# Optimization experiments

Hardware: AMD Instinct MI355X
Metric: run time of the kernel (lower is better)

Reference implementation:

```python
import jax, jax.numpy as jnp
import numpy as np

B, S, H, D = 4, 1024, 16, 64
DIM = H * D          # 1024
FF_INNER = 4 * DIM   # 4096
ROT_BASE = 1000.0


def _l2norm(x):
    # F.normalize(p=2, dim=-1): x / max(||x||_2, 1e-12)
    n = jnp.linalg.norm(x, axis=-1, keepdims=True)
    return x / jnp.maximum(n, 1e-12)


def _rmsnorm(x):
    return x * jax.lax.rsqrt(jnp.mean(x * x, axis=-1, keepdims=True) + jnp.finfo(jnp.float32).eps)


def _rope_tables(seq, d, base):
    inv_freq = base ** (-(jnp.arange(0, d, 2, dtype=jnp.float32) / d))
    freqs = jnp.outer(jnp.arange(seq, dtype=jnp.float32), inv_freq)  # [S, D/2]
    # original caches cos/sin in bfloat16
    cos = jnp.cos(freqs).astype(jnp.bfloat16)[None, :, None, :]
    sin = jnp.sin(freqs).astype(jnp.bfloat16)[None, :, None, :]
    return cos, sin


def _rope(x, cos, sin):
    d = x.shape[3] // 2
    x1, x2 = x[..., :d], x[..., d:]
    y1 = x1 * cos + x2 * sin
    y2 = -x1 * sin + x2 * cos
    return jnp.concatenate([y1, y2], axis=3).astype(x.dtype)


def setup_inputs() -> dict:
    key = jax.random.key(0)
    ks = jax.random.split(key, 12)
    w = lambda k, shp: 0.02 * jax.random.normal(k, shp, dtype=jnp.float32)
    inp = {
        'h_states': jax.random.normal(ks[0], (B, S, DIM), dtype=jnp.float32),
        'attention_mask': jnp.tril(jnp.ones((S, S), dtype=jnp.float32))[None].repeat(B, axis=0),
        'Wq': w(ks[1], (DIM, DIM)), 'Wk': w(ks[2], (DIM, DIM)), 'Wv': w(ks[3], (DIM, DIM)),
        'WqB': w(ks[4], (DIM, DIM)), 'WkB': w(ks[5], (DIM, DIM)),
        'Wo': w(ks[6], (DIM, DIM)), 'bo': jnp.zeros((DIM,), jnp.float32),
        'Wff_in': w(ks[7], (DIM, 2 * FF_INNER)), 'bff_in': jnp.zeros((2 * FF_INNER,), jnp.float32),
        'Wff_out': w(ks[8], (FF_INNER, DIM)), 'bff_out': jnp.zeros((DIM,), jnp.float32),
        'learnedlambda': jnp.asarray(1.0, jnp.float32),
        'l2normscale': jnp.log(jnp.asarray(float(S) ** 2 - float(S), jnp.float32)),
    }
    return inp


def reference(h_states, attention_mask, Wq, Wk, Wv, WqB, WkB, Wo, bo,
              Wff_in, bff_in, Wff_out, bff_out, learnedlambda, l2normscale):
    inner = _rmsnorm(h_states)                               # layerwisenorm (rmsnorm, no affine)
    scale = D ** -0.5

    def proj(Wm):
        return (inner @ Wm).reshape(B, S, H, D)
    q, k, v = proj(Wq), proj(Wk), proj(Wv)
    bq, bk = proj(WqB), proj(WkB)

    cos, sin = _rope_tables(S, D, ROT_BASE)
    q = _rope(_l2norm(q), cos, sin)
    k = _rope(_l2norm(k), cos, sin)
    bq = _rope(_l2norm(bq), cos, sin)
    bk = _rope(_l2norm(bk), cos, sin)

    # main branch: causal softmax attention, scale=1, scaled by learned l2normscale
    scores = jnp.einsum('bihd,bjhd->bhij', q, k)             # [B,H,S,S]
    causal = jnp.tril(jnp.ones((S, S), dtype=bool))
    scores = jnp.where(causal, scores, -jnp.inf)
    attn = jax.nn.softmax(scores, axis=-1)
    y = l2normscale * jnp.einsum('bhij,bjhd->bihd', attn, v)  # [B,S,H,D]

    # bias branch: softmax-free masked scores @ ones == row-sum broadcast over D
    bscores = jnp.einsum('bihd,bjhd->bhij', bq, bk) * scale
    bscores = bscores * attention_mask[:, None, :, :]
    brow = bscores.sum(axis=-1)                               # [B,H,S]
    y = y + jnp.transpose(brow, (0, 2, 1))[..., None]         # broadcast over D

    attn_out = y.reshape(B, S, DIM) @ Wo + bo

    # SwiGLU FFN: chunk -> x, gate; silu(gate) * x
    u = inner @ Wff_in + bff_in
    xh, gate = jnp.split(u, 2, axis=-1)
    dense_out = (jax.nn.silu(gate) * xh) @ Wff_out + bff_out

    return h_states * learnedlambda + dense_out + attn_out
```

## Files before the change

kernel.cpp:

```cpp
#include <hip/hip_runtime.h>
#include <stdint.h>
#include <math.h>

typedef float f32x4 __attribute__((ext_vector_type(4)));
typedef short s16x8 __attribute__((ext_vector_type(8)));
typedef unsigned short bfu;

#define AS1q const __attribute__((address_space(1))) void*
#define AS3q __attribute__((address_space(3))) void*

static __device__ __forceinline__ float bf2f(bfu v) {
  return __uint_as_float(((unsigned int)v) << 16);
}
static __device__ __forceinline__ bfu f2bf(float f) {
  unsigned int u = __float_as_uint(f);
  return (bfu)((u + 0x7fffu + ((u >> 16) & 1u)) >> 16);
}

struct PreArgs {
  const float* w5[5];
  const float* Wffin;
  const float* Wffout;
  const float* Wo;
  const float* h;
  bfu* wt5; bfu* wtfi; bfu* wtfoc;
  bfu* cosb; bfu* sinb; bfu* inner;
};
__global__ __launch_bounds__(256) void prologue_k(PreArgs a) {
  __shared__ float shmem[32 * 33];
  int id = blockIdx.x;
  if (id < 18432) {
    const float* W; bfu* Wt; int K, N, dstride, dofs, mode, nb, kb;
    if (id < 5120) {
      int z = id >> 10, rem = id & 1023;
      W = a.w5[z]; Wt = a.wt5 + ((size_t)z << 20);
      K = 1024; N = 1024; dstride = 1024; dofs = 0; mode = 0;
      nb = (rem & 31) << 5; kb = (rem >> 5) << 5;
    } else if (id < 13312) {
      int id2 = id - 5120;
      W = a.Wffin; Wt = a.wtfi; K = 1024; N = 8192; dstride = 1024; dofs = 0; mode = 1;
      nb = (id2 & 255) << 5; kb = (id2 >> 8) << 5;
    } else if (id < 17408) {
      int id3 = id - 13312;
      W = a.Wffout; Wt = a.wtfoc; K = 4096; N = 1024; dstride = 5120; dofs = 0; mode = 2;
      nb = (id3 & 31) << 5; kb = (id3 >> 5) << 5;
    } else {
      int id4 = id - 17408;
      W = a.Wo; Wt = a.wtfoc; K = 1024; N = 1024; dstride = 5120; dofs = 4096; mode = 2;
      nb = (id4 & 31) << 5; kb = (id4 >> 5) << 5;
    }
    float (*t)[33] = reinterpret_cast<float(*)[33]>(shmem);
    int tx = threadIdx.x & 31, ty = threadIdx.x >> 5;
#pragma unroll
    for (int i = 0; i < 4; i++) {
      int r = ty + i * 8;
      t[r][tx] = W[(size_t)(kb + r) * N + nb + tx];
    }
    __syncthreads();
#pragma unroll
    for (int i = 0; i < 4; i++) {
      int r = ty + i * 8;
      int n = nb + r;
      int nd = n;
      if (mode == 1) { int j = n & 4095, isg = n >> 12; nd = ((j >> 4) << 5) | (isg << 4) | (j & 15); }
      int k = kb + tx;
      int kp = (mode == 2) ? (((k >> 5) << 5) | ((k & 15) << 1) | ((k >> 4) & 1)) : k;
      Wt[(size_t)nd * dstride + dofs + kp] = f2bf(t[tx][r]);
    }
  } else if (id < 18560) {
    int idx = (id - 18432) * 256 + threadIdx.x;
    int s = idx >> 5, i = idx & 31;
    float f = powf(1000.0f, -(float)i / 32.0f);
    float fr = (float)s * f;
    a.cosb[idx] = f2bf(cosf(fr));
    a.sinb[idx] = f2bf(sinf(fr));
  } else {
    int row = id - 18560;
    const float* hr = a.h + (size_t)row * 1024;
    f32x4 x = *reinterpret_cast<const f32x4*>(hr + threadIdx.x * 4);
    float ss = x[0] * x[0] + x[1] * x[1] + x[2] * x[2] + x[3] * x[3];
    for (int off = 32; off; off >>= 1) ss += __shfl_down(ss, off);
    int wave = threadIdx.x >> 6, lane = threadIdx.x & 63;
    if (lane == 0) shmem[wave] = ss;
    __syncthreads();
    float tot = shmem[0] + shmem[1] + shmem[2] + shmem[3];
    float r = rsqrtf(tot * (1.0f / 1024.0f) + 1.1920929e-07f);
    bfu* o = a.inner + (size_t)row * 1024 + threadIdx.x * 4;
    o[0] = f2bf(x[0] * r); o[1] = f2bf(x[1] * r);
    o[2] = f2bf(x[2] * r); o[3] = f2bf(x[3] * r);
  }
}

template <int EPI>
__global__ __launch_bounds__(512, 2) void gemm256p(const bfu* __restrict__ A, const bfu* __restrict__ Bt,
                                                   bfu* __restrict__ outB,
                                                   const float* __restrict__ bias,
                                                   int M, int N, int K, int rbm, int rbn) {
  __shared__ __align__(16) char lds[131072];
  int nbx = N >> 8;
  int c = blockIdx.x & 7, rr = blockIdx.x >> 3;
  int ca = nbx / rbn;
  int bn0 = (c % ca) * rbn, bm0 = (c / ca) * rbm;
  int bm = bm0 + rr / rbn, bn = bn0 + rr % rbn;
  int tid = threadIdx.x, w = tid >> 6, lane = tid & 63;
  int wm = w >> 2, wn = w & 3;
  int g = lane >> 4, l15 = lane & 15;
  int NT = K >> 6;
  int NI = NT >> 1;

  f32x4 acc[8][4];
#pragma unroll
  for (int m = 0; m < 8; m++)
#pragma unroll
    for (int n = 0; n < 4; n++) acc[m][n] = (f32x4){0.f, 0.f, 0.f, 0.f};

  s16x8 af[4][2];
  s16x8 bfr[4][2];

  auto stage = [&](int mat, int kt, int hf) {
    if (kt >= NT) return;
    int d = kt & 1;
    const bfu* s0 = (mat == 0) ? A : Bt;
    int rowbase = ((mat == 0) ? bm : bn) * 256 + hf * 128;
    int k0 = kt << 6;
    char* base = lds + d * 65536 + mat * 32768 + hf * 16384;
#pragma unroll
    for (int r = 0; r < 2; r++) {
      int L = r * 512 + tid;
      int row = L >> 3, cc = L & 7;
      int kc = cc ^ (row & 7);
      const bfu* src = s0 + (size_t)(rowbase + row) * K + k0 + kc * 8;
      char* dst = base + r * 8192 + w * 1024;
      __builtin_amdgcn_global_load_lds((AS1q)src, (AS3q)dst, 16, 0, 0);
    }
  };

  auto ldA = [&](int d, int mh) {
    const char* base = lds + d * 65536 + wm * 16384;
#pragma unroll
    for (int mm = 0; mm < 4; mm++) {
      int row = mh * 64 + mm * 16 + l15;
#pragma unroll
      for (int ks = 0; ks < 2; ks++)
        af[mm][ks] = *reinterpret_cast<const s16x8*>(
            base + row * 128 + (((ks * 4 + g) ^ (row & 7)) << 4));
    }
  };
  auto ldB2 = [&](int d, int nh) {
    const char* base = lds + d * 65536 + 32768 + (wn >> 1) * 16384;
#pragma unroll
    for (int nn = 0; nn < 2; nn++) {
      int row = (wn & 1) * 64 + (nh * 2 + nn) * 16 + l15;
#pragma unroll
      for (int ks = 0; ks < 2; ks++)
        bfr[nh * 2 + nn][ks] = *reinterpret_cast<const s16x8*>(
            base + row * 128 + (((ks * 4 + g) ^ (row & 7)) << 4));
    }
  };
  auto mfma_q = [&](int mh, int nh) {
    asm volatile("s_waitcnt lgkmcnt(0)" ::: "memory");
    __builtin_amdgcn_sched_barrier(0);
    __builtin_amdgcn_s_barrier();
    __builtin_amdgcn_s_setprio(1);
#pragma unroll
    for (int mm = 0; mm < 4; mm++)
#pragma unroll
      for (int nn = 0; nn < 2; nn++) {
        int n = nh * 2 + nn, m = mh * 4 + mm;
#pragma unroll
        for (int ks = 0; ks < 2; ks++)
          acc[m][n] = __builtin_amdgcn_mfma_f32_16x16x32_bf16(af[mm][ks], bfr[n][ks], acc[m][n], 0, 0, 0);
      }
    __builtin_amdgcn_s_setprio(0);
    __builtin_amdgcn_sched_barrier(0);
  };

  stage(1, 0, 0); stage(0, 0, 0); stage(0, 0, 1); stage(1, 0, 1);
  stage(1, 1, 0); stage(1, 1, 1);
  asm volatile("s_waitcnt vmcnt(4)" ::: "memory");
  __builtin_amdgcn_s_barrier();
  __builtin_amdgcn_sched_barrier(0);

  for (int i = 0; i < NI; i++) {
    int t0 = 2 * i, t1 = 2 * i + 1;
    bool last = (i == NI - 1);
    ldA(0, 0); ldB2(0, 0);
    stage(0, t1, 0);
    mfma_q(0, 0);
    ldB2(0, 1);
    stage(0, t1, 1);
    mfma_q(0, 1);
    ldA(0, 1);
    stage(1, t0 + 2, 0);
    mfma_q(1, 0);
    stage(1, t0 + 2, 1);
    mfma_q(1, 1);
    if (last) { asm volatile("s_waitcnt vmcnt(0)" ::: "memory"); }
    else      { asm volatile("s_waitcnt vmcnt(4)" ::: "memory"); }
    __builtin_amdgcn_s_barrier();
    __builtin_amdgcn_sched_barrier(0);
    ldA(1, 0); ldB2(1, 0);
    stage(0, t0 + 2, 0);
    mfma_q(0, 0);
    ldB2(1, 1);
    stage(0, t0 + 2, 1);
    mfma_q(0, 1);
    ldA(1, 1);
    stage(1, t1 + 2, 0);
    mfma_q(1, 0);
    stage(1, t1 + 2, 1);
    mfma_q(1, 1);
    asm volatile("s_waitcnt vmcnt(4)" ::: "memory");
    __builtin_amdgcn_s_barrier();
    __builtin_amdgcn_sched_barrier(0);
  }

  int j0 = (bn * 8 + wn * 2) * 16 + l15;
  float bx0 = bias[j0], bg0 = bias[j0 + 4096];
  float bx1 = bias[j0 + 16], bg1 = bias[j0 + 16 + 4096];
  int cb = (bn * 4 + wn) * 32 + 2 * l15;
#pragma unroll
  for (int m = 0; m < 8; m++) {
#pragma unroll
    for (int r = 0; r < 4; r++) {
      int row = bm * 256 + wm * 128 + m * 16 + g * 4 + r;
      float xh0 = acc[m][0][r] + bx0, gt0 = acc[m][1][r] + bg0;
      float xh1 = acc[m][2][r] + bx1, gt1 = acc[m][3][r] + bg1;
      float s0 = gt0 / (1.0f + __expf(-gt0)) * xh0;
      float s1 = gt1 / (1.0f + __expf(-gt1)) * xh1;
      unsigned int pk = (unsigned int)f2bf(s0) | ((unsigned int)f2bf(s1) << 16);
      *reinterpret_cast<unsigned int*>(outB + (size_t)row * 5120 + cb) = pk;
    }
  }
}

__global__ __launch_bounds__(256, 3) void gemm128p(const bfu* __restrict__ A, const bfu* __restrict__ Bt,
                                                   bfu* __restrict__ qb, bfu* __restrict__ kb,
                                                   bfu* __restrict__ vb,
                                                   bfu* __restrict__ bqh, bfu* __restrict__ bkh,
                                                   const bfu* __restrict__ ct, const bfu* __restrict__ st,
                                                   int M, int N, int K, int rbm, int rbn) {
  __shared__ __align__(16) char lds[49152];
  int nbx = N >> 7;
  int c = blockIdx.x & 7, rr = blockIdx.x >> 3;
  int ca = nbx / rbn;
  int bn0 = (c % ca) * rbn, bm0 = (c / ca) * rbm;
  int bm = bm0 + rr / rbn, bn = bn0 + rr % rbn;
  int tid = threadIdx.x, w = tid >> 6, lane = tid & 63;
  int wm = w >> 1, wn = w & 1;
  int g = lane >> 4, l15 = lane & 15;
  int NT = K >> 5;

  f32x4 acc[4][4];
#pragma unroll
  for (int m = 0; m < 4; m++)
#pragma unroll
    for (int n = 0; n < 4; n++) acc[m][n] = (f32x4){0.f, 0.f, 0.f, 0.f};

  auto stage = [&](int buf, int t) {
    int k0 = t << 5;
#pragma unroll
    for (int r = 0; r < 2; r++) {
      int L = r * 256 + tid;
      int row = L >> 2, cc = L & 3;
      int kc = cc ^ (row & 3);
      const bfu* srcA = A + (size_t)(bm * 128 + row) * K + k0 + kc * 8;
      char* dstA = lds + buf * 16384 + r * 4096 + w * 1024;
      __builtin_amdgcn_global_load_lds((AS1q)srcA, (AS3q)dstA, 16, 0, 0);
      const bfu* srcB = Bt + (size_t)(bn * 128 + row) * K + k0 + kc * 8;
      char* dstB = lds + buf * 16384 + 8192 + r * 4096 + w * 1024;
      __builtin_amdgcn_global_load_lds((AS1q)srcB, (AS3q)dstB, 16, 0, 0);
    }
  };

  stage(0, 0); stage(1, 1);
  asm volatile("s_waitcnt vmcnt(4)" ::: "memory");
  __builtin_amdgcn_s_barrier();
  __builtin_amdgcn_sched_barrier(0);

  int bc = 0;
  for (int t = 0; t < NT; t++) {
    int bs = bc + 2; if (bs >= 3) bs -= 3;
    if (t + 2 < NT) stage(bs, t + 2);
    const char* la = lds + bc * 16384;
    const char* lb = la + 8192;
    s16x8 af[4], bfr[4];
#pragma unroll
    for (int m = 0; m < 4; m++) {
      int row = wm * 64 + m * 16 + l15;
      af[m] = *reinterpret_cast<const s16x8*>(la + row * 64 + ((g ^ (row & 3)) << 4));
    }
#pragma unroll
    for (int n = 0; n < 4; n++) {
      int row = wn * 64 + n * 16 + l15;
      bfr[n] = *reinterpret_cast<const s16x8*>(lb + row * 64 + ((g ^ (row & 3)) << 4));
    }
    asm volatile("s_waitcnt lgkmcnt(0)" ::: "memory");
    __builtin_amdgcn_sched_barrier(0);
    __builtin_amdgcn_s_setprio(1);
#pragma unroll
    for (int m = 0; m < 4; m++)
#pragma unroll
      for (int n = 0; n < 4; n++)
        acc[m][n] = __builtin_amdgcn_mfma_f32_16x16x32_bf16(af[m], bfr[n], acc[m][n], 0, 0, 0);
    __builtin_amdgcn_s_setprio(0);
    __builtin_amdgcn_sched_barrier(0);
    if (t < NT - 2) { asm volatile("s_waitcnt vmcnt(4)" ::: "memory"); }
    else            { asm volatile("s_waitcnt vmcnt(0)" ::: "memory"); }
    __builtin_amdgcn_s_barrier();
    __builtin_amdgcn_sched_barrier(0);
    bc++; if (bc == 3) bc = 0;
  }

  int which = bn >> 3;
  int hh = (bn & 7) * 2 + wn;
#pragma unroll
  for (int m = 0; m < 4; m++) {
#pragma unroll
    for (int r = 0; r < 4; r++) {
      int row = bm * 128 + wm * 64 + m * 16 + g * 4 + r;
      int s = row & 1023, b = row >> 10;
      float a0 = acc[m][0][r], a1 = acc[m][1][r];
      float a2 = acc[m][2][r], a3 = acc[m][3][r];
      if (which == 2) {
        unsigned long long pk =
            (unsigned long long)((unsigned int)f2bf(a0) | ((unsigned int)f2bf(a1) << 16)) |
            ((unsigned long long)((unsigned int)f2bf(a2) | ((unsigned int)f2bf(a3) << 16)) << 32);
        *reinterpret_cast<unsigned long long*>(
            vb + ((size_t)(b * 1024 + s) << 10) + (hh << 6) + (l15 << 2)) = pk;
      } else {
        float ss = a0 * a0 + a1 * a1 + a2 * a2 + a3 * a3;
        ss += __shfl_xor(ss, 1); ss += __shfl_xor(ss, 2);
        ss += __shfl_xor(ss, 4); ss += __shfl_xor(ss, 8);
        float inv = 1.0f / fmaxf(sqrtf(ss), 1e-12f);
        float xn0 = a0 * inv, xn1 = a1 * inv, xn2 = a2 * inv, xn3 = a3 * inv;
        float c0 = bf2f(ct[(s << 5) + l15]),      s0v = bf2f(st[(s << 5) + l15]);
        float c1 = bf2f(ct[(s << 5) + 16 + l15]), s1v = bf2f(st[(s << 5) + 16 + l15]);
        float o0 = xn0 * c0 + xn2 * s0v;
        float o1 = xn1 * c1 + xn3 * s1v;
        float o2 = xn2 * c0 - xn0 * s0v;
        float o3 = xn3 * c1 - xn1 * s1v;
        unsigned long long pk =
            (unsigned long long)((unsigned int)f2bf(o0) | ((unsigned int)f2bf(o1) << 16)) |
            ((unsigned long long)((unsigned int)f2bf(o2) | ((unsigned int)f2bf(o3) << 16)) << 32);
        size_t base = ((((size_t)((b << 4) + hh) << 10) + s) << 6) + (l15 << 2);
        bfu* dst = (which == 0) ? qb : (which == 1) ? kb : (which == 3) ? bqh : bkh;
        *reinterpret_cast<unsigned long long*>(dst + base) = pk;
      }
    }
  }
}

__global__ __launch_bounds__(256, 3) void gemm128f(const bfu* __restrict__ A, const bfu* __restrict__ Bt,
                                                   float* __restrict__ out,
                                                   const float* __restrict__ b1,
                                                   const float* __restrict__ b2,
                                                   const float* __restrict__ lam,
                                                   const float* __restrict__ h,
                                                   int M, int N, int K, int rbm, int rbn) {
  __shared__ __align__(16) char lds[49152];
  int nbx = N >> 7;
  int c = blockIdx.x & 7, rr = blockIdx.x >> 3;
  int ca = nbx / rbn;
  int bn0 = (c % ca) * rbn, bm0 = (c / ca) * rbm;
  int bm = bm0 + rr / rbn, bn = bn0 + rr % rbn;
  int tid = threadIdx.x, w = tid >> 6, lane = tid & 63;
  int wm = w >> 1, wn = w & 1;
  int g = lane >> 4, l15 = lane & 15;
  int NT = K >> 5;

  f32x4 acc[4][4];
#pragma unroll
  for (int m = 0; m < 4; m++)
#pragma unroll
    for (int n = 0; n < 4; n++) acc[m][n] = (f32x4){0.f, 0.f, 0.f, 0.f};

  auto stage = [&](int buf, int t) {
    int k0 = t << 5;
#pragma unroll
    for (int r = 0; r < 2; r++) {
      int L = r * 256 + tid;
      int row = L >> 2, cc = L & 3;
      int kc = cc ^ (row & 3);
      const bfu* srcA = A + (size_t)(bm * 128 + row) * K + k0 + kc * 8;
      char* dstA = lds + buf * 16384 + r * 4096 + w * 1024;
      __builtin_amdgcn_global_load_lds((AS1q)srcA, (AS3q)dstA, 16, 0, 0);
      const bfu* srcB = Bt + (size_t)(bn * 128 + row) * K + k0 + kc * 8;
      char* dstB = lds + buf * 16384 + 8192 + r * 4096 + w * 1024;
      __builtin_amdgcn_global_load_lds((AS1q)srcB, (AS3q)dstB, 16, 0, 0);
    }
  };

  stage(0, 0); stage(1, 1);
  asm volatile("s_waitcnt vmcnt(4)" ::: "memory");
  __builtin_amdgcn_s_barrier();
  __builtin_amdgcn_sched_barrier(0);

  int bc = 0;
  for (int t = 0; t < NT; t++) {
    int bs = bc + 2; if (bs >= 3) bs -= 3;
    if (t + 2 < NT) stage(bs, t + 2);
    const char* la = lds + bc * 16384;
    const char* lb = la + 8192;
    s16x8 af[4], bfr[4];
#pragma unroll
    for (int m = 0; m < 4; m++) {
      int row = wm * 64 + m * 16 + l15;
      af[m] = *reinterpret_cast<const s16x8*>(la + row * 64 + ((g ^ (row & 3)) << 4));
    }
#pragma unroll
    for (int n = 0; n < 4; n++) {
      int row = wn * 64 + n * 16 + l15;
      bfr[n] = *reinterpret_cast<const s16x8*>(lb + row * 64 + ((g ^ (row & 3)) << 4));
    }
    asm volatile("s_waitcnt lgkmcnt(0)" ::: "memory");
    __builtin_amdgcn_sched_barrier(0);
    __builtin_amdgcn_s_setprio(1);
#pragma unroll
    for (int m = 0; m < 4; m++)
#pragma unroll
      for (int n = 0; n < 4; n++)
        acc[m][n] = __builtin_amdgcn_mfma_f32_16x16x32_bf16(af[m], bfr[n], acc[m][n], 0, 0, 0);
    __builtin_amdgcn_s_setprio(0);
    __builtin_amdgcn_sched_barrier(0);
    if (t < NT - 2) { asm volatile("s_waitcnt vmcnt(4)" ::: "memory"); }
    else            { asm volatile("s_waitcnt vmcnt(0)" ::: "memory"); }
    __builtin_amdgcn_s_barrier();
    __builtin_amdgcn_sched_barrier(0);
    bc++; if (bc == 3) bc = 0;
  }

  float lv = lam[0];
#pragma unroll
  for (int m = 0; m < 4; m++) {
    int row = bm * 128 + wm * 64 + m * 16 + g * 4;
#pragma unroll
    for (int n = 0; n < 4; n++) {
      int col = bn * 128 + wn * 64 + n * 16 + l15;
      float bb = b1[col] + b2[col];
#pragma unroll
      for (int r = 0; r < 4; r++) {
        size_t o = (size_t)(row + r) * 1024 + col;
        out[o] = acc[m][n][r] + bb + lv * h[o];
      }
    }
  }
}

__global__ __launch_bounds__(256) void vtrans(const bfu* __restrict__ vb, bfu* __restrict__ vT) {
  __shared__ bfu t[64][66];
  int bh = blockIdx.y, stile = blockIdx.x;
  int b = bh >> 4, h = bh & 15;
  int s0 = stile << 6;
  for (int ii = threadIdx.x; ii < 4096; ii += 256) {
    int r = ii >> 6, d = ii & 63;
    t[r][d] = vb[(size_t)(b * 1024 + s0 + r) * 1024 + (h << 6) + d];
  }
  __syncthreads();
  for (int ii = threadIdx.x; ii < 4096; ii += 256) {
    int d = ii >> 6, sc = ii & 63;
    int psrc = ((d & 15) << 2) | (d >> 4);
    vT[((size_t)(bh * 64 + d) << 10) + s0 + sc] = t[sc][psrc];
  }
}

__global__ __launch_bounds__(512) void brow_all(const bfu* __restrict__ bq, const bfu* __restrict__ bk,
                                                float* __restrict__ brow) {
  __shared__ float csums[8][64];
  int bh = blockIdx.x;
  int wave = threadIdx.x >> 6, lane = threadIdx.x & 63;
  size_t base = ((size_t)bh * 1024 + wave * 128) * 64 + lane;
  float s = 0.f;
  for (int j = 0; j < 128; j++) s += bf2f(bk[base + (size_t)j * 64]);
  csums[wave][lane] = s;
  __syncthreads();
  float p = 0.f;
  for (int cc = 0; cc < wave; cc++) p += csums[cc][lane];
  for (int j = 0; j < 128; j++) {
    p += bf2f(bk[base + (size_t)j * 64]);
    float t = bf2f(bq[base + (size_t)j * 64]) * p;
#pragma unroll
    for (int m2 = 1; m2 < 64; m2 <<= 1) t += __shfl_xor(t, m2);
    if (lane == 0) brow[bh * 1024 + wave * 128 + j] = 0.125f * t;
  }
}

__global__ __launch_bounds__(256) void flash_k(const bfu* __restrict__ q, const bfu* __restrict__ k,
                                               const bfu* __restrict__ vT,
                                               const float* __restrict__ brow,
                                               const float* __restrict__ l2p,
                                               bfu* __restrict__ y) {
  __shared__ __align__(16) bfu P[4][2][16][72];
  int id = blockIdx.x;
  int sub = id & 255;
  int qt = (id >> 8) ? 7 - (sub >> 6) : (sub >> 6);
  int bh = sub & 63;
  int wave = threadIdx.x >> 6, lane = threadIdx.x & 63;
  int g = lane >> 4, l15 = lane & 15;
  const size_t bhofs = (size_t)bh << 16;
  int rt0 = qt * 128 + wave * 32;

  s16x8 aq[2][2];
#pragma unroll
  for (int m = 0; m < 2; m++)
#pragma unroll
    for (int ks = 0; ks < 2; ks++)
      aq[m][ks] = *reinterpret_cast<const s16x8*>(
          q + bhofs + (size_t)(rt0 + m * 16 + l15) * 64 + ks * 32 + g * 8);

  f32x4 O[2][4];
  float mr[2][4], lr[2][4];
#pragma unroll
  for (int m = 0; m < 2; m++)
#pragma unroll
    for (int r = 0; r < 4; r++) { O[m][r] = (f32x4){0.f, 0.f, 0.f, 0.f}; mr[m][r] = -3.0e38f; lr[m][r] = 0.f; }

  s16x8 kA[4][2], kB[4][2];
  auto loadK = [&](s16x8 (&kd)[4][2], int jt) {
#pragma unroll
    for (int nt = 0; nt < 4; nt++)
#pragma unroll
      for (int ks = 0; ks < 2; ks++)
        kd[nt][ks] = *reinterpret_cast<const s16x8*>(
            k + bhofs + (size_t)(jt * 64 + nt * 16 + l15) * 64 + ks * 32 + g * 8);
  };

  int njt = 2 * qt + 2;
  loadK(kA, 0);

  auto body = [&](int jt, s16x8 (&kc)[4][2], s16x8 (&kn)[4][2], bool pf) {
    s16x8 vv[4][2];
#pragma unroll
    for (int nt = 0; nt < 4; nt++)
#pragma unroll
      for (int ks = 0; ks < 2; ks++)
        vv[nt][ks] = *reinterpret_cast<const s16x8*>(
            vT + ((size_t)(bh * 64 + nt * 16 + l15) << 10) + jt * 64 + ks * 32 + g * 8);

    bool act[2] = { jt * 64 <= rt0 + 15, jt * 64 <= rt0 + 31 };
    f32x4 sfr[2][4];
#pragma unroll
    for (int m = 0; m < 2; m++) {
      if (!act[m]) continue;
#pragma unroll
      for (int nt = 0; nt < 4; nt++) {
        sfr[m][nt] = (f32x4){0.f, 0.f, 0.f, 0.f};
#pragma unroll
        for (int ks = 0; ks < 2; ks++)
          sfr[m][nt] = __builtin_amdgcn_mfma_f32_16x16x32_bf16(aq[m][ks], kc[nt][ks], sfr[m][nt], 0, 0, 0);
      }
    }
    if (pf) loadK(kn, jt + 1);

#pragma unroll
    for (int m = 0; m < 2; m++) {
      if (!act[m]) continue;
      int rtm = rt0 + m * 16;
      if (jt * 64 + 63 > rtm) {
#pragma unroll
        for (int ntn = 0; ntn < 4; ntn++)
#pragma unroll
          for (int r = 0; r < 4; r++)
            if (jt * 64 + ntn * 16 + l15 > rtm + g * 4 + r) sfr[m][ntn][r] = -1e30f;
      }
      float alpha[4];
#pragma unroll
      for (int r = 0; r < 4; r++) {
        float v = fmaxf(fmaxf(sfr[m][0][r], sfr[m][1][r]), fmaxf(sfr[m][2][r], sfr[m][3][r]));
#pragma unroll
        for (int m2 = 1; m2 < 16; m2 <<= 1) v = fmaxf(v, __shfl_xor(v, m2));
        float mn = fmaxf(mr[m][r], v);
        alpha[r] = __expf(mr[m][r] - mn);
        mr[m][r] = mn;
      }
#pragma unroll
      for (int r = 0; r < 4; r++) {
        float rs = 0.f;
#pragma unroll
        for (int ntn = 0; ntn < 4; ntn++) {
          float e = __expf(sfr[m][ntn][r] - mr[m][r]);
          rs += e;
          P[wave][m][g * 4 + r][ntn * 16 + l15] = f2bf(e);
        }
#pragma unroll
        for (int m2 = 1; m2 < 16; m2 <<= 1) rs += __shfl_xor(rs, m2);
        lr[m][r] = lr[m][r] * alpha[r] + rs;
#pragma unroll
        for (int ntn = 0; ntn < 4; ntn++) O[m][ntn][r] *= alpha[r];
      }
    }
    asm volatile("s_waitcnt lgkmcnt(0)" ::: "memory");
    __builtin_amdgcn_sched_barrier(0);
#pragma unroll
    for (int m = 0; m < 2; m++) {
      if (!act[m]) continue;
      s16x8 pa[2];
#pragma unroll
      for (int ks = 0; ks < 2; ks++)
        pa[ks] = *reinterpret_cast<const s16x8*>(&P[wave][m][l15][ks * 32 + g * 8]);
#pragma unroll
      for (int nt = 0; nt < 4; nt++)
#pragma unroll
        for (int ks = 0; ks < 2; ks++)
          O[m][nt] = __builtin_amdgcn_mfma_f32_16x16x32_bf16(pa[ks], vv[nt][ks], O[m][nt], 0, 0, 0);
    }
  };

  for (int jt = 0; jt < njt; jt += 2) {
    body(jt, kA, kB, true);
    body(jt + 1, kB, kA, jt + 2 < njt);
  }

  float l2ns = l2p[0];
  int b = bh >> 4, hq = bh & 15;
#pragma unroll
  for (int m = 0; m < 2; m++)
#pragma unroll
    for (int r = 0; r < 4; r++) {
      int rowg = rt0 + m * 16 + g * 4 + r;
      float br = brow[bh * 1024 + rowg];
      float sc = l2ns / lr[m][r];
      float v0 = O[m][0][r] * sc + br;
      float v1 = O[m][1][r] * sc + br;
      float v2 = O[m][2][r] * sc + br;
      float v3 = O[m][3][r] * sc + br;
      unsigned int p01 = (unsigned int)f2bf(v0) | ((unsigned int)f2bf(v1) << 16);
      unsigned int p23 = (unsigned int)f2bf(v2) | ((unsigned int)f2bf(v3) << 16);
      size_t base = (size_t)(b * 1024 + rowg) * 5120 + 4096 + hq * 64;
      *reinterpret_cast<unsigned int*>(y + base + 2 * l15) = p01;
      *reinterpret_cast<unsigned int*>(y + base + 32 + 2 * l15) = p23;
    }
}

extern "C" void kernel_launch(void* const* d_in, const int* in_sizes, int n_in,
                              void* d_out, int out_size, void* d_ws, size_t ws_size,
                              hipStream_t stream) {
  const float* h      = (const float*)d_in[0];
  const float* Wq     = (const float*)d_in[2];
  const float* Wk     = (const float*)d_in[3];
  const float* Wv     = (const float*)d_in[4];
  const float* WqB    = (const float*)d_in[5];
  const float* WkB    = (const float*)d_in[6];
  const float* Wo     = (const float*)d_in[7];
  const float* bo     = (const float*)d_in[8];
  const float* Wffin  = (const float*)d_in[9];
  const float* bffin  = (const float*)d_in[10];
  const float* Wffout = (const float*)d_in[11];
  const float* bffout = (const float*)d_in[12];
  const float* lam    = (const float*)d_in[13];
  const float* l2ns   = (const float*)d_in[14];
  float* out = (float*)d_out;

  char* ws = (char*)d_ws;
  size_t off = 0;
  auto alloc = [&](size_t bytes) { void* p = ws + off; off += bytes; return p; };
  bfu* wt5   = (bfu*)alloc(5ull * 1024 * 1024 * 2);
  bfu* wtfi  = (bfu*)alloc(8192ull * 1024 * 2);
  bfu* wtfoc = (bfu*)alloc(1024ull * 5120 * 2);
  bfu* cosb  = (bfu*)alloc(1024ull * 32 * 2);
  bfu* sinb  = (bfu*)alloc(1024ull * 32 * 2);
  bfu* inner = (bfu*)alloc(4096ull * 1024 * 2);
  bfu* qb    = (bfu*)alloc(64ull * 1024 * 64 * 2);
  bfu* kb    = (bfu*)alloc(64ull * 1024 * 64 * 2);
  bfu* vb    = (bfu*)alloc(4096ull * 1024 * 2);
  bfu* vtb   = (bfu*)alloc(64ull * 1024 * 64 * 2);
  bfu* bqh   = (bfu*)alloc(64ull * 1024 * 64 * 2);
  bfu* bkh   = (bfu*)alloc(64ull * 1024 * 64 * 2);
  float* browb = (float*)alloc(64ull * 1024 * 4);
  bfu* AB    = (bfu*)alloc(4096ull * 5120 * 2);

  PreArgs pa;
  pa.w5[0] = Wq; pa.w5[1] = Wk; pa.w5[2] = Wv; pa.w5[3] = WqB; pa.w5[4] = WkB;
  pa.Wffin = Wffin; pa.Wffout = Wffout; pa.Wo = Wo; pa.h = h;
  pa.wt5 = wt5; pa.wtfi = wtfi; pa.wtfoc = wtfoc;
  pa.cosb = cosb; pa.sinb = sinb; pa.inner = inner;
  prologue_k<<<dim3(22656), 256, 0, stream>>>(pa);

  gemm128p<<<dim3(1280), 256, 0, stream>>>(inner, wt5, qb, kb, vb, bqh, bkh, cosb, sinb,
                                           4096, 5120, 1024, 32, 5);

  vtrans<<<dim3(16, 64), 256, 0, stream>>>(vb, vtb);
  brow_all<<<dim3(64), 512, 0, stream>>>(bqh, bkh, browb);

  flash_k<<<dim3(512), 256, 0, stream>>>(qb, kb, vtb, browb, l2ns, AB);

  gemm256p<1><<<dim3(512), 512, 0, stream>>>(inner, wtfi, AB, bffin,
                                             4096, 8192, 1024, 8, 8);

  gemm128f<<<dim3(256), 256, 0, stream>>>(AB, wtfoc, out, bffout, bo, lam, h,
                                          4096, 1024, 5120, 8, 4);
}
```

Before: 348.8 us.

## Fuse V transpose into QKV GEMM epilogue and deepen K-tile of output GEMM

The QKV projection GEMM now writes V directly in transposed [b,h,d,s] layout by staging the tile through LDS in its epilogue, which removes the separate vtrans kernel and the intermediate V buffer round trip. Separately, the final output GEMM (gemm128f) doubles its K-step from 32 to 64, doubling LDS per stage to 96KB with a wider XOR swizzle, so there are fewer barrier iterations per tile. The larger LDS footprint lowers occupancy for gemm128f, and the new epilogue's layout has to match the permuted d ordering that vtrans used to apply.

```diff
diff --git a/kernel.cpp b/kernel.cpp
--- a/kernel.cpp
+++ b/kernel.cpp
@@ -236,7 +236,7 @@
 
 __global__ __launch_bounds__(256, 3) void gemm128p(const bfu* __restrict__ A, const bfu* __restrict__ Bt,
                                                    bfu* __restrict__ qb, bfu* __restrict__ kb,
-                                                   bfu* __restrict__ vb,
+                                                   bfu* __restrict__ vT,
                                                    bfu* __restrict__ bqh, bfu* __restrict__ bkh,
                                                    const bfu* __restrict__ ct, const bfu* __restrict__ st,
                                                    int M, int N, int K, int rbm, int rbn) {
@@ -314,21 +314,40 @@
 
   int which = bn >> 3;
   int hh = (bn & 7) * 2 + wn;
-#pragma unroll
-  for (int m = 0; m < 4; m++) {
-#pragma unroll
-    for (int r = 0; r < 4; r++) {
-      int row = bm * 128 + wm * 64 + m * 16 + g * 4 + r;
-      int s = row & 1023, b = row >> 10;
-      float a0 = acc[m][0][r], a1 = acc[m][1][r];
-      float a2 = acc[m][2][r], a3 = acc[m][3][r];
-      if (which == 2) {
-        unsigned long long pk =
-            (unsigned long long)((unsigned int)f2bf(a0) | ((unsigned int)f2bf(a1) << 16)) |
-            ((unsigned long long)((unsigned int)f2bf(a2) | ((unsigned int)f2bf(a3) << 16)) << 32);
-        *reinterpret_cast<unsigned long long*>(
-            vb + ((size_t)(b * 1024 + s) << 10) + (hh << 6) + (l15 << 2)) = pk;
-      } else {
+  if (which == 2) {
+    bfu* lv = reinterpret_cast<bfu*>(lds);
+#pragma unroll
+    for (int m = 0; m < 4; m++) {
+#pragma unroll
+      for (int r = 0; r < 4; r++) {
+        int sl = wm * 64 + m * 16 + g * 4 + r;
+#pragma unroll
+        for (int j = 0; j < 4; j++) {
+          int d = j * 16 + l15;
+          lv[(wn * 64 + d) * 136 + sl] = f2bf(acc[m][j][r]);
+        }
+      }
+    }
+    __syncthreads();
+    int b = bm >> 3, h0 = (bn & 7) * 2;
+#pragma unroll
+    for (int i = 0; i < 8; i++) {
+      int linear = i * 256 + tid;
+      int hw = linear >> 10, rem = linear & 1023;
+      int d = rem >> 4, sl8 = (rem & 15) << 3;
+      s16x8 v8 = *reinterpret_cast<const s16x8*>(&lv[(hw * 64 + d) * 136 + sl8]);
+      size_t dstofs = (((size_t)((b << 4) + h0 + hw) << 6) + d) * 1024 + (bm & 7) * 128 + sl8;
+      *reinterpret_cast<s16x8*>(vT + dstofs) = v8;
+    }
+  } else {
+#pragma unroll
+    for (int m = 0; m < 4; m++) {
+#pragma unroll
+      for (int r = 0; r < 4; r++) {
+        int row = bm * 128 + wm * 64 + m * 16 + g * 4 + r;
+        int s = row & 1023, b = row >> 10;
+        float a0 = acc[m][0][r], a1 = acc[m][1][r];
+        float a2 = acc[m][2][r], a3 = acc[m][3][r];
         float ss = a0 * a0 + a1 * a1 + a2 * a2 + a3 * a3;
         ss += __shfl_xor(ss, 1); ss += __shfl_xor(ss, 2);
         ss += __shfl_xor(ss, 4); ss += __shfl_xor(ss, 8);
@@ -358,7 +377,7 @@
                                                    const float* __restrict__ lam,
                                                    const float* __restrict__ h,
                                                    int M, int N, int K, int rbm, int rbn) {
-  __shared__ __align__(16) char lds[49152];
+  __shared__ __align__(16) char lds[98304];
   int nbx = N >> 7;
   int c = blockIdx.x & 7, rr = blockIdx.x >> 3;
   int ca = nbx / rbn;
@@ -367,7 +386,7 @@
   int tid = threadIdx.x, w = tid >> 6, lane = tid & 63;
   int wm = w >> 1, wn = w & 1;
   int g = lane >> 4, l15 = lane & 15;
-  int NT = K >> 5;
+  int NT = K >> 6;
 
   f32x4 acc[4][4];
 #pragma unroll
@@ -376,23 +395,29 @@
     for (int n = 0; n < 4; n++) acc[m][n] = (f32x4){0.f, 0.f, 0.f, 0.f};
 
   auto stage = [&](int buf, int t) {
-    int k0 = t << 5;
-#pragma unroll
-    for (int r = 0; r < 2; r++) {
+    int k0 = t << 6;
+#pragma unroll
+    for (int r = 0; r < 4; r++) {
       int L = r * 256 + tid;
-      int row = L >> 2, cc = L & 3;
-      int kc = cc ^ (row & 3);
+      int row = L >> 3, cc = L & 7;
+      int kc = cc ^ (row & 7);
       const bfu* srcA = A + (size_t)(bm * 128 + row) * K + k0 + kc * 8;
-      char* dstA = lds + buf * 16384 + r * 4096 + w * 1024;
+      char* dstA = lds + buf * 32768 + r * 4096 + w * 1024;
       __builtin_amdgcn_global_load_lds((AS1q)srcA, (AS3q)dstA, 16, 0, 0);
+    }
+#pragma unroll
+    for (int r = 0; r < 4; r++) {
+      int L = r * 256 + tid;
+      int row = L >> 3, cc = L & 7;
+      int kc = cc ^ (row & 7);
       const bfu* srcB = Bt + (size_t)(bn * 128 + row) * K + k0 + kc * 8;
-      char* dstB = lds + buf * 16384 + 8192 + r * 4096 + w * 1024;
+      char* dstB = lds + buf * 32768 + 16384 + r * 4096 + w * 1024;
       __builtin_amdgcn_global_load_lds((AS1q)srcB, (AS3q)dstB, 16, 0, 0);
     }
   };
 
   stage(0, 0); stage(1, 1);
-  asm volatile("s_waitcnt vmcnt(4)" ::: "memory");
+  asm volatile("s_waitcnt vmcnt(8)" ::: "memory");
   __builtin_amdgcn_s_barrier();
   __builtin_amdgcn_sched_barrier(0);
 
@@ -400,18 +425,24 @@
   for (int t = 0; t < NT; t++) {
     int bs = bc + 2; if (bs >= 3) bs -= 3;
     if (t + 2 < NT) stage(bs, t + 2);
-    const char* la = lds + bc * 16384;
-    const char* lb = la + 8192;
-    s16x8 af[4], bfr[4];
+    const char* la = lds + bc * 32768;
+    const char* lb = la + 16384;
+    s16x8 af[4][2], bfr[4][2];
 #pragma unroll
     for (int m = 0; m < 4; m++) {
       int row = wm * 64 + m * 16 + l15;
-      af[m] = *reinterpret_cast<const s16x8*>(la + row * 64 + ((g ^ (row & 3)) << 4));
+#pragma unroll
+      for (int ks = 0; ks < 2; ks++)
+        af[m][ks] = *reinterpret_cast<const s16x8*>(
+            la + row * 128 + (((ks * 4 + g) ^ (row & 7)) << 4));
     }
 #pragma unroll
     for (int n = 0; n < 4; n++) {
       int row = wn * 64 + n * 16 + l15;
-      bfr[n] = *reinterpret_cast<const s16x8*>(lb + row * 64 + ((g ^ (row & 3)) << 4));
+#pragma unroll
+      for (int ks = 0; ks < 2; ks++)
+        bfr[n][ks] = *reinterpret_cast<const s16x8*>(
+            lb + row * 128 + (((ks * 4 + g) ^ (row & 7)) << 4));
     }
     asm volatile("s_waitcnt lgkmcnt(0)" ::: "memory");
     __builtin_amdgcn_sched_barrier(0);
@@ -420,10 +451,12 @@
     for (int m = 0; m < 4; m++)
 #pragma unroll
       for (int n = 0; n < 4; n++)
-        acc[m][n] = __builtin_amdgcn_mfma_f32_16x16x32_bf16(af[m], bfr[n], acc[m][n], 0, 0, 0);
+#pragma unroll
+        for (int ks = 0; ks < 2; ks++)
+          acc[m][n] = __builtin_amdgcn_mfma_f32_16x16x32_bf16(af[m][ks], bfr[n][ks], acc[m][n], 0, 0, 0);
     __builtin_amdgcn_s_setprio(0);
     __builtin_amdgcn_sched_barrier(0);
-    if (t < NT - 2) { asm volatile("s_waitcnt vmcnt(4)" ::: "memory"); }
+    if (t < NT - 2) { asm volatile("s_waitcnt vmcnt(8)" ::: "memory"); }
     else            { asm volatile("s_waitcnt vmcnt(0)" ::: "memory"); }
     __builtin_amdgcn_s_barrier();
     __builtin_amdgcn_sched_barrier(0);
@@ -444,23 +477,6 @@
         out[o] = acc[m][n][r] + bb + lv * h[o];
       }
     }
-  }
-}
-
-__global__ __launch_bounds__(256) void vtrans(const bfu* __restrict__ vb, bfu* __restrict__ vT) {
-  __shared__ bfu t[64][66];
-  int bh = blockIdx.y, stile = blockIdx.x;
-  int b = bh >> 4, h = bh & 15;
-  int s0 = stile << 6;
-  for (int ii = threadIdx.x; ii < 4096; ii += 256) {
-    int r = ii >> 6, d = ii & 63;
-    t[r][d] = vb[(size_t)(b * 1024 + s0 + r) * 1024 + (h << 6) + d];
-  }
-  __syncthreads();
-  for (int ii = threadIdx.x; ii < 4096; ii += 256) {
-    int d = ii >> 6, sc = ii & 63;
-    int psrc = ((d & 15) << 2) | (d >> 4);
-    vT[((size_t)(bh * 64 + d) << 10) + s0 + sc] = t[sc][psrc];
   }
 }
 
@@ -662,7 +678,6 @@
   bfu* inner = (bfu*)alloc(4096ull * 1024 * 2);
   bfu* qb    = (bfu*)alloc(64ull * 1024 * 64 * 2);
   bfu* kb    = (bfu*)alloc(64ull * 1024 * 64 * 2);
-  bfu* vb    = (bfu*)alloc(4096ull * 1024 * 2);
   bfu* vtb   = (bfu*)alloc(64ull * 1024 * 64 * 2);
   bfu* bqh   = (bfu*)alloc(64ull * 1024 * 64 * 2);
   bfu* bkh   = (bfu*)alloc(64ull * 1024 * 64 * 2);
@@ -676,10 +691,9 @@
   pa.cosb = cosb; pa.sinb = sinb; pa.inner = inner;
   prologue_k<<<dim3(22656), 256, 0, stream>>>(pa);
 
-  gemm128p<<<dim3(1280), 256, 0, stream>>>(inner, wt5, qb, kb, vb, bqh, bkh, cosb, sinb,
+  gemm128p<<<dim3(1280), 256, 0, stream>>>(inner, wt5, qb, kb, vtb, bqh, bkh, cosb, sinb,
                                            4096, 5120, 1024, 32, 5);
 
-  vtrans<<<dim3(16, 64), 256, 0, stream>>>(vb, vtb);
   brow_all<<<dim3(64), 512, 0, stream>>>(bqh, bkh, browb);
 
   flash_k<<<dim3(512), 256, 0, stream>>>(qb, kb, vtb, browb, l2ns, AB);
```

After: 322.6 us (median of 3 runs). 7.5% less time.
